# Kernel tuning notes

Measured on AMD Instinct MI355X. Metric: run time of the kernel, lower is better.

## Reference

```python
import jax, jax.numpy as jnp
import numpy as np

B, T, C, HEAD = 4, 4096, 2048, 128
ROPE_BASE = 10000.0


def _rope_tables(T, dim):
    # precompute_freqs_cis: freqs = 1/base^(2i/dim), angles = t * freqs
    inv_freq = 1.0 / (ROPE_BASE ** (np.arange(0, dim, 2, dtype=np.float32) / dim))
    angles = np.arange(T, dtype=np.float32)[:, None] * inv_freq[None, :]  # [T, dim/2]
    return jnp.asarray(np.cos(angles)), jnp.asarray(np.sin(angles))


def _apply_rope(x, cos, sin):
    # x: [B, T, D]; interleaved complex pairs (x[2i], x[2i+1]) rotated by angle
    B_, T_, D = x.shape
    xr = x.reshape(B_, T_, D // 2, 2)
    x1, x2 = xr[..., 0], xr[..., 1]
    o1 = x1 * cos - x2 * sin
    o2 = x1 * sin + x2 * cos
    return jnp.stack([o1, o2], axis=-1).reshape(B_, T_, D)


def setup_inputs() -> dict:
    key0 = jax.random.key(0)
    k1, k2, k3, k4 = jax.random.split(key0, 4)
    x = jax.random.normal(k1, (B, T, C), dtype=jnp.float32)
    key = jax.random.normal(k2, (B, T, HEAD), dtype=jnp.float32)
    value = jax.random.normal(k3, (B, T, HEAD), dtype=jnp.float32)
    w_q = jax.random.normal(k4, (HEAD, C), dtype=jnp.float32) * 0.02
    return {"x": x, "key": key, "value": value, "w_q": w_q}


def reference(x, key, value, w_q):
    # query projection (nn.Linear, no bias)
    q = jnp.einsum('btc,dc->btd', x, w_q)  # [B, T, HEAD]
    cos, sin = _rope_tables(T, HEAD)
    # apply_rotary_emb(key, query) returns (key_rot, query_rot); then
    # query, key = (key_rot, query_rot) and wei = key @ query^T == q_rot @ k_rot^T
    q_rot = _apply_rope(q, cos, sin)
    k_rot = _apply_rope(key, cos, sin)
    scale = HEAD ** -0.5
    wei = jnp.einsum('btd,bsd->bts', q_rot, k_rot) * scale  # [B, T, T]
    causal = jnp.tril(jnp.ones((T, T), dtype=bool))
    wei = jnp.where(causal, wei, -jnp.inf)
    wei = jax.nn.softmax(wei, axis=-1)
    # dropout is identity in eval / p=0
    return jnp.einsum('bts,bsd->btd', wei, value)  # [B, T, HEAD]
```

## Files before the change

kernel.cpp:

```cpp
#include <hip/hip_runtime.h>
#include <hip/hip_bf16.h>

#define TSEQ  4096
#define NBATCH 4
#define CDIM  2048
#define DH    128

typedef __bf16 bf16x8 __attribute__((ext_vector_type(8)));
typedef float  f32x4  __attribute__((ext_vector_type(4)));
typedef unsigned short u16x8 __attribute__((ext_vector_type(8)));
typedef unsigned       u32x4 __attribute__((ext_vector_type(4)));
typedef unsigned short u16;

__device__ __forceinline__ u16 f2bf(float f) {
  union { float f; unsigned u; } v; v.f = f;
  unsigned r = (v.u + 0x7FFFu + ((v.u >> 16) & 1u)) >> 16;
  return (u16)r;
}
__device__ __forceinline__ float bf2f(u16 h) {
  union { unsigned u; float f; } v; v.u = ((unsigned)h) << 16;
  return v.f;
}
__device__ __forceinline__ bf16x8 ld_bf8(const u16* p) {
  return __builtin_bit_cast(bf16x8, *(const u16x8*)p);
}
__device__ __forceinline__ unsigned pk2(float lo, float hi) {
  float2 f; f.x = lo; f.y = hi;
  __hip_bfloat162 h = __float22bfloat162_rn(f);
  unsigned r; __builtin_memcpy(&r, &h, 4);
  return r;
}
__device__ __forceinline__ u16x8 cvt8u(float4 a, float4 b) {
  u32x4 u;
  u[0] = pk2(a.x, a.y); u[1] = pk2(a.z, a.w);
  u[2] = pk2(b.x, b.y); u[3] = pk2(b.z, b.w);
  return __builtin_bit_cast(u16x8, u);
}

template<int CTRL>
__device__ __forceinline__ float dppmv(float x) {
  return __builtin_bit_cast(float,
    __builtin_amdgcn_update_dpp(0, __builtin_bit_cast(int, x), CTRL, 0xF, 0xF, true));
}
__device__ __forceinline__ float red_max16(float v) {
  v = fmaxf(v, dppmv<0xB1>(v));
  v = fmaxf(v, dppmv<0x4E>(v));
  v = fmaxf(v, dppmv<0x124>(v));
  v = fmaxf(v, dppmv<0x128>(v));
  return v;
}
__device__ __forceinline__ float red_sum16(float v) {
  v += dppmv<0xB1>(v);
  v += dppmv<0x4E>(v);
  v += dppmv<0x124>(v);
  v += dppmv<0x128>(v);
  return v;
}

__device__ __forceinline__ int unit_base(int Q) {
  int a = Q >> 2, bq = Q & 3;
  return 2 * a * (a + 1) + bq * (a + 1);
}

__global__ __launch_bounds__(256) void k_prep(const float* __restrict__ w, u16* __restrict__ wbf,
                                              const float* __restrict__ key, u16* __restrict__ krot,
                                              const float* __restrict__ value, u16* __restrict__ vt,
                                              float* __restrict__ ct, float* __restrict__ st) {
  __shared__ u16 S[128 * 66];
  int bid = blockIdx.x;
  int tid = threadIdx.x;
  if (bid < 256) {
    int i = bid * 256 + tid;
    const float4 v = *(const float4*)(w + (size_t)i * 4);
    uint2 o; o.x = pk2(v.x, v.y); o.y = pk2(v.z, v.w);
    *(uint2*)(wbf + (size_t)i * 4) = o;
  } else if (bid < 1280) {
    int i = (bid - 256) * 256 + tid;
    int p = i & 63;
    int t = i >> 6;
    float inv = powf(10000.0f, -(float)p / 64.0f);
    float ang = (float)t * inv;
    float s, c; sincosf(ang, &s, &c);
    ct[i] = c; st[i] = s;
  } else if (bid < 5376) {
    int g = (bid - 1280) * 256 + tid;
    int p = g & 63;
    int row = g >> 6;
    int t = row & (TSEQ - 1);
    const float2 kv = *(const float2*)(key + (size_t)row * DH + 2 * p);
    float inv = powf(10000.0f, -(float)p / 64.0f);
    float ang = (float)t * inv;
    float s, c; sincosf(ang, &s, &c);
    *(unsigned*)(krot + (size_t)row * DH + 2 * p) = pk2(kv.x * c - kv.y * s, kv.x * s + kv.y * c);
  } else {
    int vb = bid - 5376;
    int b = vb >> 6;
    int t0 = (vb & 63) * 64;
    int d = (tid & 31) * 4;
    int tl0 = tid >> 5;
#pragma unroll
    for (int i = 0; i < 8; ++i) {
      int tl = tl0 + i * 8;
      const float4 val = *(const float4*)(value + ((size_t)(b * TSEQ + t0 + tl)) * DH + d);
      S[(d + 0) * 66 + tl] = f2bf(val.x);
      S[(d + 1) * 66 + tl] = f2bf(val.y);
      S[(d + 2) * 66 + tl] = f2bf(val.z);
      S[(d + 3) * 66 + tl] = f2bf(val.w);
    }
    __syncthreads();
#pragma unroll
    for (int i = 0; i < 16; ++i) {
      int idx = tid + i * 256;
      int dd = idx >> 5;
      int tw = (idx & 31) * 2;
      unsigned lo = S[dd * 66 + tw];
      unsigned hi = S[dd * 66 + tw + 1];
      *(unsigned*)(vt + ((size_t)(b * DH + dd)) * TSEQ + t0 + tw) = lo | (hi << 16);
    }
  }
}

__global__ __launch_bounds__(256, 2) void k_qproj(const float* __restrict__ x,
                                                  const u16* __restrict__ wbf,
                                                  const float* __restrict__ ct,
                                                  const float* __restrict__ st,
                                                  u16* __restrict__ qrot) {
  __shared__ u16 Al[16 * 32 * 8];
  int bid = blockIdx.x;
  int tid = threadIdx.x;
  int w = tid >> 6;
  int lane = tid & 63;
  int l15 = lane & 15;
  int quad = lane >> 4;
  int m0 = bid * 32;

  int srow = tid >> 3;
  int c16 = (tid & 7) * 16;
  int chunk0 = (tid & 7) * 2;
  const float* xg = x + (size_t)(m0 + srow) * CDIM + c16;

  f32x4 acc[2][2];
#pragma unroll
  for (int mt = 0; mt < 2; ++mt)
#pragma unroll
    for (int nt = 0; nt < 2; ++nt) acc[mt][nt] = (f32x4){0.f, 0.f, 0.f, 0.f};

  float4 pa[4];
#pragma unroll
  for (int i = 0; i < 4; ++i) pa[i] = *(const float4*)(xg + i * 4);

  for (int it = 0; it < CDIM / 128; ++it) {
    u16x8 lo = cvt8u(pa[0], pa[1]);
    u16x8 hi = cvt8u(pa[2], pa[3]);
    __syncthreads();
    *(u16x8*)&Al[(chunk0 * 32 + srow) * 8] = lo;
    *(u16x8*)&Al[((chunk0 + 1) * 32 + srow) * 8] = hi;
    __syncthreads();
    if (it + 1 < CDIM / 128) {
      const float* xn = xg + (size_t)(it + 1) * 128;
#pragma unroll
      for (int i = 0; i < 4; ++i) pa[i] = *(const float4*)(xn + i * 4);
    }
    int k0 = it * 128;
#pragma unroll
    for (int ks = 0; ks < 4; ++ks) {
      bf16x8 af[2];
#pragma unroll
      for (int mt = 0; mt < 2; ++mt)
        af[mt] = ld_bf8(&Al[(((ks * 4 + quad) * 32) + mt * 16 + l15) * 8]);
#pragma unroll
      for (int nt = 0; nt < 2; ++nt) {
        bf16x8 bfrag = ld_bf8(wbf + (size_t)(w * 32 + nt * 16 + l15) * CDIM + k0 + ks * 32 + quad * 8);
#pragma unroll
        for (int mt = 0; mt < 2; ++mt)
          acc[mt][nt] = __builtin_amdgcn_mfma_f32_16x16x32_bf16(af[mt], bfrag, acc[mt][nt], 0, 0, 0);
      }
    }
  }

  const float scale = 0.08838834764831845f;
#pragma unroll
  for (int mt = 0; mt < 2; ++mt)
#pragma unroll
    for (int nt = 0; nt < 2; ++nt) {
      int dcol = w * 32 + nt * 16 + l15;
      int p = dcol >> 1;
#pragma unroll
      for (int r = 0; r < 4; ++r) {
        int m = m0 + mt * 16 + quad * 4 + r;
        int t = m & (TSEQ - 1);
        float val = acc[mt][nt][r];
        float partner = __shfl_xor(val, 1, 64);
        float c = ct[t * 64 + p];
        float s = st[t * 64 + p];
        float o = (lane & 1) ? (val * c + partner * s) : (val * c - partner * s);
        qrot[(size_t)m * DH + dcol] = f2bf(o * scale);
      }
    }
}

__global__ __launch_bounds__(256, 2) void k_attn(const u16* __restrict__ qrot,
                                                 const u16* __restrict__ krot,
                                                 const u16* __restrict__ vt,
                                                 u16* __restrict__ Opart,
                                                 float2* __restrict__ ml) {
  __shared__ u16 Kl[16 * 64 * 8];
  __shared__ u16 Vl[8 * 128 * 8];
  __shared__ u16 Pl[4 * 32 * 72];

  int bid = blockIdx.x;
  int b = bid / 144;
  int u = bid - b * 144;
  int Q = 0;
#pragma unroll 1
  for (int q = 31; q >= 0; --q) {
    if (unit_base(q) <= u) { Q = q; break; }
  }
  int kc = u - unit_base(Q);
  int nkt = 2 * Q + 2;
  int kt0 = kc * 8;
  int kt1 = min(kt0 + 8, nkt);
  int m0 = Q * 128;

  int tid = threadIdx.x;
  int w = tid >> 6;
  int lane = tid & 63;
  int l15 = lane & 15;
  int quad = lane >> 4;
  u16* pw = Pl + w * 32 * 72;

  int rK = tid & 63;   int jgK = tid >> 6;
  int dV = tid & 127;  int hV = tid >> 7;

  const u16* kb = krot + (size_t)b * TSEQ * DH;
  const u16* vb = vt + (size_t)b * DH * TSEQ;

  bf16x8 qf[2][4];
#pragma unroll
  for (int mt = 0; mt < 2; ++mt) {
    const u16* qb = qrot + ((size_t)(b * TSEQ + m0 + mt * 64 + w * 16 + l15)) * DH + quad * 8;
#pragma unroll
    for (int c = 0; c < 4; ++c) qf[mt][c] = ld_bf8(qb + c * 32);
  }

  f32x4 o_acc[2][8];
#pragma unroll
  for (int mt = 0; mt < 2; ++mt)
#pragma unroll
    for (int i = 0; i < 8; ++i) o_acc[mt][i] = (f32x4){0.f, 0.f, 0.f, 0.f};
  float m_st[2][4], l_st[2][4];
#pragma unroll
  for (int mt = 0; mt < 2; ++mt)
#pragma unroll
    for (int r = 0; r < 4; ++r) { m_st[mt][r] = -INFINITY; l_st[mt][r] = 0.f; }

  u16x8 kr[4], vr[4];
  {
    const u16* ks = kb + (size_t)(kt0 * 64 + rK) * DH + jgK * 32;
    const u16* vs = vb + (size_t)dV * TSEQ + kt0 * 64 + hV * 32;
#pragma unroll
    for (int i = 0; i < 4; ++i) { kr[i] = *(const u16x8*)(ks + i * 8); vr[i] = *(const u16x8*)(vs + i * 8); }
  }

  for (int kt = kt0; kt < kt1; ++kt) {
    __syncthreads();
#pragma unroll
    for (int i = 0; i < 4; ++i) {
      *(u16x8*)&Kl[((jgK * 4 + i) * 64 + rK) * 8] = kr[i];
      *(u16x8*)&Vl[((hV * 4 + i) * 128 + dV) * 8] = vr[i];
    }
    __syncthreads();
    if (kt + 1 < kt1) {
      const u16* ks = kb + (size_t)((kt + 1) * 64 + rK) * DH + jgK * 32;
      const u16* vs = vb + (size_t)dV * TSEQ + (kt + 1) * 64 + hV * 32;
#pragma unroll
      for (int i = 0; i < 4; ++i) { kr[i] = *(const u16x8*)(ks + i * 8); vr[i] = *(const u16x8*)(vs + i * 8); }
    }

    f32x4 s[2][4];
#pragma unroll
    for (int mt = 0; mt < 2; ++mt)
#pragma unroll
      for (int nt = 0; nt < 4; ++nt) s[mt][nt] = (f32x4){0.f, 0.f, 0.f, 0.f};
#pragma unroll
    for (int c = 0; c < 4; ++c)
#pragma unroll
      for (int nt = 0; nt < 4; ++nt) {
        bf16x8 kf = ld_bf8(&Kl[((c * 4 + quad) * 64 + nt * 16 + l15) * 8]);
#pragma unroll
        for (int mt = 0; mt < 2; ++mt)
          s[mt][nt] = __builtin_amdgcn_mfma_f32_16x16x32_bf16(qf[mt][c], kf, s[mt][nt], 0, 0, 0);
      }

    if (kt * 64 >= m0) {
#pragma unroll
      for (int mt = 0; mt < 2; ++mt)
#pragma unroll
        for (int nt = 0; nt < 4; ++nt)
#pragma unroll
          for (int r = 0; r < 4; ++r) {
            int key_g = kt * 64 + nt * 16 + l15;
            int row_g = m0 + mt * 64 + w * 16 + quad * 4 + r;
            if (key_g > row_g) s[mt][nt][r] = -INFINITY;
          }
    }

    float alpha[2][4];
    int chg = 0;
#pragma unroll
    for (int mt = 0; mt < 2; ++mt)
#pragma unroll
      for (int r = 0; r < 4; ++r) {
        float rm = fmaxf(fmaxf(s[mt][0][r], s[mt][1][r]), fmaxf(s[mt][2][r], s[mt][3][r]));
        rm = red_max16(rm);
        float mn = fmaxf(m_st[mt][r], rm);
        float al = __expf(m_st[mt][r] - mn);
        m_st[mt][r] = mn;
        float ps = 0.f;
#pragma unroll
        for (int nt = 0; nt < 4; ++nt) {
          float pv = __expf(s[mt][nt][r] - mn);
          s[mt][nt][r] = pv;
          ps += pv;
        }
        ps = red_sum16(ps);
        l_st[mt][r] = l_st[mt][r] * al + ps;
        alpha[mt][r] = al;
        chg |= (al != 1.0f);
      }
    if (__any(chg)) {
#pragma unroll
      for (int mt = 0; mt < 2; ++mt)
#pragma unroll
        for (int nt = 0; nt < 8; ++nt)
#pragma unroll
          for (int r = 0; r < 4; ++r) o_acc[mt][nt][r] *= alpha[mt][r];
    }

#pragma unroll
    for (int mt = 0; mt < 2; ++mt)
#pragma unroll
      for (int nt = 0; nt < 4; ++nt)
#pragma unroll
        for (int r = 0; r < 4; ++r)
          pw[(mt * 16 + quad * 4 + r) * 72 + nt * 16 + l15] = f2bf(s[mt][nt][r]);

#pragma unroll
    for (int c2 = 0; c2 < 2; ++c2) {
      bf16x8 pf[2];
#pragma unroll
      for (int mt = 0; mt < 2; ++mt)
        pf[mt] = ld_bf8(pw + (mt * 16 + l15) * 72 + c2 * 32 + quad * 8);
#pragma unroll
      for (int nt = 0; nt < 8; ++nt) {
        bf16x8 vf = ld_bf8(&Vl[((c2 * 4 + quad) * 128 + nt * 16 + l15) * 8]);
#pragma unroll
        for (int mt = 0; mt < 2; ++mt)
          o_acc[mt][nt] = __builtin_amdgcn_mfma_f32_16x16x32_bf16(pf[mt], vf, o_acc[mt][nt], 0, 0, 0);
      }
    }
  }

  u16* op = Opart + (size_t)bid * (128 * 128);
#pragma unroll
  for (int mt = 0; mt < 2; ++mt)
#pragma unroll
    for (int nt = 0; nt < 8; ++nt)
#pragma unroll
      for (int r = 0; r < 4; ++r)
        op[(mt * 64 + w * 16 + quad * 4 + r) * 128 + nt * 16 + l15] = f2bf(o_acc[mt][nt][r]);
  if (l15 == 0) {
#pragma unroll
    for (int mt = 0; mt < 2; ++mt)
#pragma unroll
      for (int r = 0; r < 4; ++r) {
        float2 p; p.x = m_st[mt][r]; p.y = l_st[mt][r];
        ml[(size_t)bid * 128 + mt * 64 + w * 16 + quad * 4 + r] = p;
      }
  }
}

__global__ __launch_bounds__(256) void k_merge(const u16* __restrict__ Opart,
                                               const float2* __restrict__ ml,
                                               float* __restrict__ out) {
  __shared__ float wgt[8][128];
  __shared__ float invL[128];
  int bid = blockIdx.x;
  int b = bid >> 5, Q = bid & 31;
  int C = (Q >> 2) + 1;
  int base = b * 144 + unit_base(Q);
  int tid = threadIdx.x;
  if (tid < 128) {
    float mv[8], lv[8];
    float M = -INFINITY;
    for (int c = 0; c < C; ++c) {
      float2 p = ml[(size_t)(base + c) * 128 + tid];
      mv[c] = p.x; lv[c] = p.y;
      M = fmaxf(M, p.x);
    }
    float L = 0.f;
    for (int c = 0; c < C; ++c) {
      float wv = __expf(mv[c] - M);
      wgt[c][tid] = wv;
      L += wv * lv[c];
    }
    invL[tid] = 1.f / L;
  }
  __syncthreads();
#pragma unroll
  for (int k = 0; k < 8; ++k) {
    int slot = tid + k * 256;
    int row = slot >> 4;
    float acc[8];
#pragma unroll
    for (int j = 0; j < 8; ++j) acc[j] = 0.f;
    for (int c = 0; c < C; ++c) {
      u16x8 v = *(const u16x8*)&Opart[(size_t)(base + c) * (128 * 128) + slot * 8];
      float wv = wgt[c][row];
#pragma unroll
      for (int j = 0; j < 8; ++j) acc[j] += wv * bf2f(v[j]);
    }
    float il = invL[row];
    float4 o0, o1;
    o0.x = acc[0] * il; o0.y = acc[1] * il; o0.z = acc[2] * il; o0.w = acc[3] * il;
    o1.x = acc[4] * il; o1.y = acc[5] * il; o1.z = acc[6] * il; o1.w = acc[7] * il;
    float* op = out + ((size_t)(b * TSEQ + Q * 128 + row)) * DH + (slot & 15) * 8;
    *(float4*)op = o0;
    *(float4*)(op + 4) = o1;
  }
}

extern "C" void kernel_launch(void* const* d_in, const int* in_sizes, int n_in,
                              void* d_out, int out_size, void* d_ws, size_t ws_size,
                              hipStream_t stream) {
  const float* x     = (const float*)d_in[0];
  const float* key   = (const float*)d_in[1];
  const float* value = (const float*)d_in[2];
  const float* w_q   = (const float*)d_in[3];
  float* out = (float*)d_out;

  char* ws = (char*)d_ws;
  u16* wbf    = (u16*)(ws);
  u16* qrot   = (u16*)(ws + (512u << 10));
  u16* krot   = (u16*)(ws + (512u << 10) + (4u << 20));
  u16* vt     = (u16*)(ws + (512u << 10) + (8u << 20));
  float* ct   = (float*)(ws + (512u << 10) + (12u << 20));
  float* st   = (float*)(ws + (512u << 10) + (13u << 20));
  u16* Opart  = (u16*)(ws + (512u << 10) + (14u << 20));
  float2* ml  = (float2*)(ws + (512u << 10) + (34u << 20));

  k_prep<<<5632, 256, 0, stream>>>(w_q, wbf, key, krot, value, vt, ct, st);
  k_qproj<<<(NBATCH * TSEQ) / 32, 256, 0, stream>>>(x, wbf, ct, st, qrot);
  k_attn<<<NBATCH * 144, 256, 0, stream>>>(qrot, krot, vt, Opart, ml);
  k_merge<<<NBATCH * 32, 256, 0, stream>>>(Opart, ml, out);
}
```

Measured before the change: 293.4 us.

## Compute RoPE inline, double-buffer x prefetch, lighter barriers and MFMA priority

The cos/sin lookup tables and their prep blocks are removed; the query projection epilogue now computes sincos per element directly. The qproj K-loop now keeps two register sets of x loads in flight and issues the next loads before the LDS barrier, to hide global-load latency. Plain __syncthreads is replaced with an LDS-only wait plus s_barrier in qproj and attention, and s_setprio is raised around the MFMA blocks in attention. The workspace layout is repacked to match. This trades table memory traffic for extra transcendental math, and adds more register pressure from the second prefetch buffer.

```diff
diff --git a/kernel.cpp b/kernel.cpp
--- a/kernel.cpp
+++ b/kernel.cpp
@@ -35,6 +35,11 @@
   u[0] = pk2(a.x, a.y); u[1] = pk2(a.z, a.w);
   u[2] = pk2(b.x, b.y); u[3] = pk2(b.z, b.w);
   return __builtin_bit_cast(u16x8, u);
+}
+
+__device__ __forceinline__ void lds_barrier() {
+  asm volatile("s_waitcnt lgkmcnt(0)" ::: "memory");
+  __builtin_amdgcn_s_barrier();
 }
 
 template<int CTRL>
@@ -64,26 +69,42 @@
 
 __global__ __launch_bounds__(256) void k_prep(const float* __restrict__ w, u16* __restrict__ wbf,
                                               const float* __restrict__ key, u16* __restrict__ krot,
-                                              const float* __restrict__ value, u16* __restrict__ vt,
-                                              float* __restrict__ ct, float* __restrict__ st) {
+                                              const float* __restrict__ value, u16* __restrict__ vt) {
   __shared__ u16 S[128 * 66];
   int bid = blockIdx.x;
   int tid = threadIdx.x;
   if (bid < 256) {
-    int i = bid * 256 + tid;
+    int vb = bid;
+    int b = vb >> 6;
+    int t0 = (vb & 63) * 64;
+    int d = (tid & 31) * 4;
+    int tl0 = tid >> 5;
+#pragma unroll
+    for (int i = 0; i < 8; ++i) {
+      int tl = tl0 + i * 8;
+      const float4 val = *(const float4*)(value + ((size_t)(b * TSEQ + t0 + tl)) * DH + d);
+      S[(d + 0) * 66 + tl] = f2bf(val.x);
+      S[(d + 1) * 66 + tl] = f2bf(val.y);
+      S[(d + 2) * 66 + tl] = f2bf(val.z);
+      S[(d + 3) * 66 + tl] = f2bf(val.w);
+    }
+    __syncthreads();
+#pragma unroll
+    for (int i = 0; i < 16; ++i) {
+      int idx = tid + i * 256;
+      int dd = idx >> 5;
+      int tw = (idx & 31) * 2;
+      unsigned lo = S[dd * 66 + tw];
+      unsigned hi = S[dd * 66 + tw + 1];
+      *(unsigned*)(vt + ((size_t)(b * DH + dd)) * TSEQ + t0 + tw) = lo | (hi << 16);
+    }
+  } else if (bid < 512) {
+    int i = (bid - 256) * 256 + tid;
     const float4 v = *(const float4*)(w + (size_t)i * 4);
     uint2 o; o.x = pk2(v.x, v.y); o.y = pk2(v.z, v.w);
     *(uint2*)(wbf + (size_t)i * 4) = o;
-  } else if (bid < 1280) {
-    int i = (bid - 256) * 256 + tid;
-    int p = i & 63;
-    int t = i >> 6;
-    float inv = powf(10000.0f, -(float)p / 64.0f);
-    float ang = (float)t * inv;
-    float s, c; sincosf(ang, &s, &c);
-    ct[i] = c; st[i] = s;
-  } else if (bid < 5376) {
-    int g = (bid - 1280) * 256 + tid;
+  } else {
+    int g = (bid - 512) * 256 + tid;
     int p = g & 63;
     int row = g >> 6;
     int t = row & (TSEQ - 1);
@@ -92,38 +113,11 @@
     float ang = (float)t * inv;
     float s, c; sincosf(ang, &s, &c);
     *(unsigned*)(krot + (size_t)row * DH + 2 * p) = pk2(kv.x * c - kv.y * s, kv.x * s + kv.y * c);
-  } else {
-    int vb = bid - 5376;
-    int b = vb >> 6;
-    int t0 = (vb & 63) * 64;
-    int d = (tid & 31) * 4;
-    int tl0 = tid >> 5;
-#pragma unroll
-    for (int i = 0; i < 8; ++i) {
-      int tl = tl0 + i * 8;
-      const float4 val = *(const float4*)(value + ((size_t)(b * TSEQ + t0 + tl)) * DH + d);
-      S[(d + 0) * 66 + tl] = f2bf(val.x);
-      S[(d + 1) * 66 + tl] = f2bf(val.y);
-      S[(d + 2) * 66 + tl] = f2bf(val.z);
-      S[(d + 3) * 66 + tl] = f2bf(val.w);
-    }
-    __syncthreads();
-#pragma unroll
-    for (int i = 0; i < 16; ++i) {
-      int idx = tid + i * 256;
-      int dd = idx >> 5;
-      int tw = (idx & 31) * 2;
-      unsigned lo = S[dd * 66 + tw];
-      unsigned hi = S[dd * 66 + tw + 1];
-      *(unsigned*)(vt + ((size_t)(b * DH + dd)) * TSEQ + t0 + tw) = lo | (hi << 16);
-    }
   }
 }
 
 __global__ __launch_bounds__(256, 2) void k_qproj(const float* __restrict__ x,
                                                   const u16* __restrict__ wbf,
-                                                  const float* __restrict__ ct,
-                                                  const float* __restrict__ st,
                                                   u16* __restrict__ qrot) {
   __shared__ u16 Al[16 * 32 * 8];
   int bid = blockIdx.x;
@@ -145,23 +139,25 @@
 #pragma unroll
     for (int nt = 0; nt < 2; ++nt) acc[mt][nt] = (f32x4){0.f, 0.f, 0.f, 0.f};
 
-  float4 pa[4];
-#pragma unroll
-  for (int i = 0; i < 4; ++i) pa[i] = *(const float4*)(xg + i * 4);
-
-  for (int it = 0; it < CDIM / 128; ++it) {
+  float4 paA[4], paB[4];
+#pragma unroll
+  for (int i = 0; i < 4; ++i) paA[i] = *(const float4*)(xg + i * 4);
+#pragma unroll
+  for (int i = 0; i < 4; ++i) paB[i] = *(const float4*)(xg + 128 + i * 4);
+
+  auto qstep = [&](float4 (&pa)[4], int itc) {
     u16x8 lo = cvt8u(pa[0], pa[1]);
     u16x8 hi = cvt8u(pa[2], pa[3]);
-    __syncthreads();
+    if (itc + 2 < CDIM / 128) {
+      const float* xn = xg + (size_t)(itc + 2) * 128;
+#pragma unroll
+      for (int i = 0; i < 4; ++i) pa[i] = *(const float4*)(xn + i * 4);
+    }
+    lds_barrier();
     *(u16x8*)&Al[(chunk0 * 32 + srow) * 8] = lo;
     *(u16x8*)&Al[((chunk0 + 1) * 32 + srow) * 8] = hi;
-    __syncthreads();
-    if (it + 1 < CDIM / 128) {
-      const float* xn = xg + (size_t)(it + 1) * 128;
-#pragma unroll
-      for (int i = 0; i < 4; ++i) pa[i] = *(const float4*)(xn + i * 4);
-    }
-    int k0 = it * 128;
+    lds_barrier();
+    int k0 = itc * 128;
 #pragma unroll
     for (int ks = 0; ks < 4; ++ks) {
       bf16x8 af[2];
@@ -176,27 +172,35 @@
           acc[mt][nt] = __builtin_amdgcn_mfma_f32_16x16x32_bf16(af[mt], bfrag, acc[mt][nt], 0, 0, 0);
       }
     }
+  };
+
+#pragma unroll 1
+  for (int ith = 0; ith < 8; ++ith) {
+    qstep(paA, 2 * ith);
+    qstep(paB, 2 * ith + 1);
   }
 
   const float scale = 0.08838834764831845f;
 #pragma unroll
-  for (int mt = 0; mt < 2; ++mt)
-#pragma unroll
-    for (int nt = 0; nt < 2; ++nt) {
-      int dcol = w * 32 + nt * 16 + l15;
-      int p = dcol >> 1;
+  for (int nt = 0; nt < 2; ++nt) {
+    int dcol = w * 32 + nt * 16 + l15;
+    int p = dcol >> 1;
+    float inv = powf(10000.0f, -(float)p / 64.0f);
+#pragma unroll
+    for (int mt = 0; mt < 2; ++mt) {
 #pragma unroll
       for (int r = 0; r < 4; ++r) {
         int m = m0 + mt * 16 + quad * 4 + r;
         int t = m & (TSEQ - 1);
+        float ang = (float)t * inv;
+        float s, c; sincosf(ang, &s, &c);
         float val = acc[mt][nt][r];
         float partner = __shfl_xor(val, 1, 64);
-        float c = ct[t * 64 + p];
-        float s = st[t * 64 + p];
         float o = (lane & 1) ? (val * c + partner * s) : (val * c - partner * s);
         qrot[(size_t)m * DH + dcol] = f2bf(o * scale);
       }
     }
+  }
 }
 
 __global__ __launch_bounds__(256, 2) void k_attn(const u16* __restrict__ qrot,
@@ -263,13 +267,13 @@
   }
 
   for (int kt = kt0; kt < kt1; ++kt) {
-    __syncthreads();
+    lds_barrier();
 #pragma unroll
     for (int i = 0; i < 4; ++i) {
       *(u16x8*)&Kl[((jgK * 4 + i) * 64 + rK) * 8] = kr[i];
       *(u16x8*)&Vl[((hV * 4 + i) * 128 + dV) * 8] = vr[i];
     }
-    __syncthreads();
+    lds_barrier();
     if (kt + 1 < kt1) {
       const u16* ks = kb + (size_t)((kt + 1) * 64 + rK) * DH + jgK * 32;
       const u16* vs = vb + (size_t)dV * TSEQ + (kt + 1) * 64 + hV * 32;
@@ -282,6 +286,7 @@
     for (int mt = 0; mt < 2; ++mt)
 #pragma unroll
       for (int nt = 0; nt < 4; ++nt) s[mt][nt] = (f32x4){0.f, 0.f, 0.f, 0.f};
+    __builtin_amdgcn_s_setprio(1);
 #pragma unroll
     for (int c = 0; c < 4; ++c)
 #pragma unroll
@@ -291,6 +296,7 @@
         for (int mt = 0; mt < 2; ++mt)
           s[mt][nt] = __builtin_amdgcn_mfma_f32_16x16x32_bf16(qf[mt][c], kf, s[mt][nt], 0, 0, 0);
       }
+    __builtin_amdgcn_s_setprio(0);
 
     if (kt * 64 >= m0) {
 #pragma unroll
@@ -351,6 +357,7 @@
 #pragma unroll
       for (int mt = 0; mt < 2; ++mt)
         pf[mt] = ld_bf8(pw + (mt * 16 + l15) * 72 + c2 * 32 + quad * 8);
+      __builtin_amdgcn_s_setprio(1);
 #pragma unroll
       for (int nt = 0; nt < 8; ++nt) {
         bf16x8 vf = ld_bf8(&Vl[((c2 * 4 + quad) * 128 + nt * 16 + l15) * 8]);
@@ -358,6 +365,7 @@
         for (int mt = 0; mt < 2; ++mt)
           o_acc[mt][nt] = __builtin_amdgcn_mfma_f32_16x16x32_bf16(pf[mt], vf, o_acc[mt][nt], 0, 0, 0);
       }
+      __builtin_amdgcn_s_setprio(0);
     }
   }
 
@@ -441,16 +449,14 @@
 
   char* ws = (char*)d_ws;
   u16* wbf    = (u16*)(ws);
-  u16* qrot   = (u16*)(ws + (512u << 10));
-  u16* krot   = (u16*)(ws + (512u << 10) + (4u << 20));
-  u16* vt     = (u16*)(ws + (512u << 10) + (8u << 20));
-  float* ct   = (float*)(ws + (512u << 10) + (12u << 20));
-  float* st   = (float*)(ws + (512u << 10) + (13u << 20));
-  u16* Opart  = (u16*)(ws + (512u << 10) + (14u << 20));
-  float2* ml  = (float2*)(ws + (512u << 10) + (34u << 20));
-
-  k_prep<<<5632, 256, 0, stream>>>(w_q, wbf, key, krot, value, vt, ct, st);
-  k_qproj<<<(NBATCH * TSEQ) / 32, 256, 0, stream>>>(x, wbf, ct, st, qrot);
+  u16* qrot   = (u16*)(ws + (1u  << 20));
+  u16* krot   = (u16*)(ws + (5u  << 20));
+  u16* vt     = (u16*)(ws + (9u  << 20));
+  u16* Opart  = (u16*)(ws + (13u << 20));
+  float2* ml  = (float2*)(ws + (32u << 20));
+
+  k_prep<<<4608, 256, 0, stream>>>(w_q, wbf, key, krot, value, vt);
+  k_qproj<<<(NBATCH * TSEQ) / 32, 256, 0, stream>>>(x, wbf, qrot);
   k_attn<<<NBATCH * 144, 256, 0, stream>>>(qrot, krot, vt, Opart, ml);
   k_merge<<<NBATCH * 32, 256, 0, stream>>>(Opart, ml, out);
 }
```

Result: no change. 292.1 us (-0.4%).
